# Kernel tuning notes

Hardware: AMD Instinct MI355X
Metric: run time of the kernel (lower is better)

## Reference

```python
import jax, jax.numpy as jnp
import numpy as np

# config (matches init_kwargs)
NA, NEN = 8, 8            # n_agents, n_enemies
NENT = NA + NEN           # n_entities
NFA, NFE = 64, 64         # state_nf_al, state_nf_en
E, A, M, HE = 64, 64, 32, 64  # entity_embed, attn_embed, mixing_embed, hypernet_embed
TD, TE = 64, 64           # task_repre_dim, task_repre_embed_dim
BS, SL = 64, 512


def setup_inputs() -> dict:
    key = jax.random.key(0)
    ks = iter(jax.random.split(key, 32))
    def rn(shape, scale=0.05):
        return jax.random.normal(next(ks), shape, dtype=jnp.float32) * scale
    return {
        "agent_qs": rn((BS, SL, NA), 1.0),
        "states": rn((BS, SL, NA * NFA + NEN * NFE), 1.0),
        "task_repre_mu": rn((BS, SL, NA, TD), 1.0),
        "ally_w": rn((NFA, E)), "ally_b": rn((E,)),
        "enemy_w": rn((NFE, E)), "enemy_b": rn((E,)),
        "q_w": rn((E, A)), "q_b": rn((A,)),
        "k_w": rn((E, A)), "k_b": rn((A,)),
        "hw1_w1": rn((E + NFA + TE, HE)), "hw1_b1": rn((HE,)),
        "hw1_w2": rn((HE, M)), "hw1_b2": rn((M,)),
        "hwf_w1": rn((E + TE, HE)), "hwf_b1": rn((HE,)),
        "hwf_w2": rn((HE, M)), "hwf_b2": rn((M,)),
        "hb1_w": rn((E + TE, M)), "hb1_b": rn((M,)),
        "v_w1": rn((E + TE, M)), "v_b1": rn((M,)),
        "v_w2": rn((M, 1)), "v_b2": rn((1,)),
        "tre_w": rn((TD, TE)), "tre_b": rn((TE,)),
    }


def reference(agent_qs, states, task_repre_mu,
              ally_w, ally_b, enemy_w, enemy_b,
              q_w, q_b, k_w, k_b,
              hw1_w1, hw1_b1, hw1_w2, hw1_b2,
              hwf_w1, hwf_b1, hwf_w2, hwf_b2,
              hb1_w, hb1_b, v_w1, v_b1, v_w2, v_b2,
              tre_w, tre_b):
    bs, sl = agent_qs.shape[:2]
    # decompose_state (state_last_action=False, state_timestep_number=False)
    ally = states[..., : NA * NFA].reshape(bs, sl, NA, NFA)      # [bs,sl,NA,NFA]
    enemy = states[..., NA * NFA:].reshape(bs, sl, NEN, NFE)     # [bs,sl,NEN,NFE]
    ally_e = ally @ ally_w + ally_b                              # [bs,sl,NA,E]
    enemy_e = enemy @ enemy_w + enemy_b                          # [bs,sl,NEN,E]
    ent = jnp.concatenate([ally_e, enemy_e], axis=2)             # [bs,sl,NENT,E]
    q = ent @ q_w + q_b                                          # [bs,sl,NENT,A]
    k = ent @ k_w + k_b
    energy = jnp.einsum('bsqa,bska->bsqk', q, k)                 # [bs,sl,NENT,NENT]
    # torch: F.softmax(energy, dim=1) on [B,n_ent,n_ent] -> softmax over query axis
    attn = jax.nn.softmax(energy, axis=2)
    # attn_out = bmm(value[B,E,n], attn[B,n,n]).mean(-1)
    attn_out = jnp.einsum('bsne,bsnk->bse', ent, attn) / NENT    # [bs,sl,E]

    mean_mu = task_repre_mu.mean(axis=-2)                        # [bs,sl,TD]
    tre = task_repre_mu @ tre_w + tre_b                          # [bs,sl,NA,TE]
    mean_tre = mean_mu @ tre_w + tre_b                           # [bs,sl,TE]

    ent_mix = jnp.concatenate([
        jnp.broadcast_to(attn_out[:, :, None, :], (bs, sl, NA, E)),
        ally, tre], axis=-1)                                     # [bs,sl,NA,E+NFA+TE]
    mix = jnp.concatenate([attn_out, mean_tre], axis=-1)         # [bs,sl,E+TE]

    w1 = jnp.abs(jax.nn.relu(ent_mix @ hw1_w1 + hw1_b1) @ hw1_w2 + hw1_b2)  # [bs,sl,NA,M]
    b1 = mix @ hb1_w + hb1_b                                     # [bs,sl,M]
    hidden = jax.nn.elu(jnp.einsum('bsn,bsnm->bsm', agent_qs, w1) + b1)     # [bs,sl,M]
    wf = jnp.abs(jax.nn.relu(mix @ hwf_w1 + hwf_b1) @ hwf_w2 + hwf_b2)      # [bs,sl,M]
    v = jax.nn.relu(mix @ v_w1 + v_b1) @ v_w2 + v_b2             # [bs,sl,1]
    q_tot = jnp.einsum('bsm,bsm->bs', hidden, wf)[..., None] + v # [bs,sl,1]
    return q_tot
```

## Files before the change

kernel.cpp:

```cpp
#include <hip/hip_runtime.h>
#include <math.h>


#define TOKS 32768

typedef __attribute__((ext_vector_type(8))) short short8;
typedef __attribute__((ext_vector_type(4))) float f32x4;

#define MFMA(a, b, c) __builtin_amdgcn_mfma_f32_16x16x32_bf16((a), (b), (c), 0, 0, 0)

#define E_CAT   0
#define E_WQKT  8192
#define E_ZBRT  13312
#define E_H1T   29696
#define E_W2T   41984
#define E_WFT   44032
#define E_BF16_TOTAL 46080
#define E_AO_US 46464

__device__ __forceinline__ unsigned short bfr(float x) {
    unsigned u = __builtin_bit_cast(unsigned, x);
    u += 0x7fffu + ((u >> 16) & 1u);
    return (unsigned short)(u >> 16);
}
__device__ __forceinline__ float bf2f(unsigned short h) {
    unsigned u = ((unsigned)h) << 16;
    return __builtin_bit_cast(float, u);
}
__device__ __forceinline__ short8 cvt8v(float4 a, float4 b) {
    short8 r;
    r[0] = (short)bfr(a.x); r[1] = (short)bfr(a.y);
    r[2] = (short)bfr(a.z); r[3] = (short)bfr(a.w);
    r[4] = (short)bfr(b.x); r[5] = (short)bfr(b.y);
    r[6] = (short)bfr(b.z); r[7] = (short)bfr(b.w);
    return r;
}
#define SWZ64(r, c)  ((((r) * 64)  + (c)) ^ (((r) & 7) << 3))
#define SWZ128(r, c) ((((r) * 128) + (c)) ^ (((r) & 7) << 3))
#define SWZ192(r, c) ((((r) * 192) + (c)) ^ (((r) & 7) << 3))

__global__ __launch_bounds__(256) void qmix_setup(
    const float* __restrict__ ally_w, const float* __restrict__ enemy_w,
    const float* __restrict__ q_w, const float* __restrict__ k_w,
    const float* __restrict__ k_b,
    const float* __restrict__ hw1_w1, const float* __restrict__ hw1_b1,
    const float* __restrict__ hw1_w2,
    const float* __restrict__ hwf_w1, const float* __restrict__ hwf_b1,
    const float* __restrict__ hwf_w2,
    const float* __restrict__ hb1_w, const float* __restrict__ hb1_b,
    const float* __restrict__ v_w1, const float* __restrict__ v_b1,
    const float* __restrict__ tre_w, const float* __restrict__ tre_b,
    unsigned short* __restrict__ wsb, float* __restrict__ wsf)
{
    int gid = blockIdx.x * 256 + threadIdx.x;
    if (gid < E_BF16_TOTAL) {
        float v = 0.f;
        int base, r, c, K;
        if (gid < E_WQKT) {
            base = E_CAT; K = 128;
            int i = gid - base; r = i >> 7; c = i & 127;
            v = (c < 64) ? ally_w[c * 64 + r] : enemy_w[(c - 64) * 64 + r];
        } else if (gid < E_ZBRT) {
            base = E_WQKT; K = 64;
            int i = gid - base; r = i >> 6; c = i & 63;
            if (r < 64) {
                for (int g = 0; g < 64; ++g) v += q_w[c * 64 + g] * k_w[r * 64 + g];
            } else if (r == 64) {
                for (int g = 0; g < 64; ++g) v += q_w[c * 64 + g] * k_b[g];
            }
        } else if (gid < E_H1T) {
            base = E_ZBRT; K = 128;
            int i = gid - base; r = i >> 7; c = i & 127;
            if (r < 64) {
                if (c < 64) v = hwf_w1[c * 64 + r];
                else for (int g = 0; g < 64; ++g) v += tre_w[(c - 64) * 64 + g] * hwf_w1[(64 + g) * 64 + r];
            } else if (r < 96) {
                int m = r - 64;
                if (c < 64) v = hb1_w[c * 32 + m];
                else for (int g = 0; g < 64; ++g) v += tre_w[(c - 64) * 64 + g] * hb1_w[(64 + g) * 32 + m];
            } else {
                int m = r - 96;
                if (c < 64) v = v_w1[c * 32 + m];
                else for (int g = 0; g < 64; ++g) v += tre_w[(c - 64) * 64 + g] * v_w1[(64 + g) * 32 + m];
            }
        } else if (gid < E_W2T) {
            base = E_H1T; K = 192;
            int i = gid - base; r = i / 192; c = i % 192;
            if (c < 64) v = hw1_w1[(64 + c) * 64 + r];
            else if (c < 128) {
                for (int g = 0; g < 64; ++g) v += tre_w[(c - 64) * 64 + g] * hw1_w1[(128 + g) * 64 + r];
            } else v = hw1_w1[(c - 128) * 64 + r];
        } else if (gid < E_WFT) {
            base = E_W2T; K = 64;
            int i = gid - base; r = i >> 6; c = i & 63;
            v = hw1_w2[c * 32 + r];
        } else {
            base = E_WFT; K = 64;
            int i = gid - base; r = i >> 6; c = i & 63;
            v = hwf_w2[c * 32 + r];
        }
        wsb[base + ((r * K + c) ^ ((r & 7) << 3))] = bfr(v);
    } else if (gid < E_BF16_TOTAL + 192) {
        int j = gid - E_BF16_TOTAL; float v;
        if (j < 64) {
            v = hw1_b1[j];
            for (int g = 0; g < 64; ++g) v += tre_b[g] * hw1_w1[(128 + g) * 64 + j];
        } else if (j < 128) {
            int e = j - 64; v = hwf_b1[e];
            for (int g = 0; g < 64; ++g) v += tre_b[g] * hwf_w1[(64 + g) * 64 + e];
        } else if (j < 160) {
            int m = j - 128; v = hb1_b[m];
            for (int g = 0; g < 64; ++g) v += tre_b[g] * hb1_w[(64 + g) * 32 + m];
        } else {
            int m = j - 160; v = v_b1[m];
            for (int g = 0; g < 64; ++g) v += tre_b[g] * v_w1[(64 + g) * 32 + m];
        }
        wsf[j] = v;
    }
}

__global__ __launch_bounds__(512) void qmix_attn(
    const float* __restrict__ states,
    const float* __restrict__ ally_b, const float* __restrict__ enemy_b,
    const unsigned short* __restrict__ wsb,
    unsigned short* __restrict__ aoG)
{
    __shared__ unsigned short sWa[13312];
    __shared__ unsigned short sE[8][1024];
    __shared__ unsigned short sT[8][1024];

    const int lane = threadIdx.x & 63;
    const int wv   = threadIdx.x >> 6;
    const int l15  = lane & 15;
    const int lg   = lane >> 4;
    const int kb   = lg * 8;
    const size_t t = (size_t)blockIdx.x * 8 + wv;

    const short8 zero8 = {0, 0, 0, 0, 0, 0, 0, 0};
    const f32x4  zero4 = {0.f, 0.f, 0.f, 0.f};

    for (int i = threadIdx.x * 8; i < 13312; i += 512 * 8)
        *(short8*)(sWa + i) = *(const short8*)(wsb + E_CAT + i);

    const int roff = (l15 < 8) ? (l15 * 64 + kb) : (512 + (l15 - 8) * 64 + kb);
    const float* p = states + t * 1024 + roff;
    float4 cur0 = *(const float4*)(p);
    float4 cur1 = *(const float4*)(p + 4);
    float4 cur2 = *(const float4*)(p + 32);
    float4 cur3 = *(const float4*)(p + 36);

    float biasEnt[4];
    #pragma unroll
    for (int nt = 0; nt < 4; ++nt) {
        int col = nt * 16 + l15;
        biasEnt[nt] = (lg < 2) ? ally_b[col] : enemy_b[col];
    }
    __syncthreads();
    const unsigned short* lCAT  = sWa;
    const unsigned short* lWQKT = sWa + 8192;

    unsigned short* E = sE[wv];
    unsigned short* T = sT[wv];

    short8 a01 = cvt8v(cur0, cur1);
    short8 a23 = cvt8v(cur2, cur3);
    const bool isally = (l15 < 8);

    f32x4 accB[4] = {zero4, zero4, zero4, zero4};
    #pragma unroll
    for (int ks = 0; ks < 4; ++ks) {
        short8 af;
        if (ks == 0)      af = isally ? a01 : zero8;
        else if (ks == 1) af = isally ? a23 : zero8;
        else if (ks == 2) af = isally ? zero8 : a01;
        else              af = isally ? zero8 : a23;
        #pragma unroll
        for (int nt = 0; nt < 4; ++nt) {
            short8 w = *(const short8*)&lCAT[SWZ128(nt * 16 + l15, ks * 32 + kb)];
            accB[nt] = MFMA(af, w, accB[nt]);
        }
    }
    float entv[4][4];
    #pragma unroll
    for (int nt = 0; nt < 4; ++nt) {
        #pragma unroll
        for (int reg = 0; reg < 4; ++reg) {
            entv[nt][reg] = accB[nt][reg] + biasEnt[nt];
            E[SWZ64(lg * 4 + reg, nt * 16 + l15)] = bfr(entv[nt][reg]);
        }
    }

    f32x4 accC[5] = {zero4, zero4, zero4, zero4, zero4};
    short8 ef0 = *(const short8*)&E[SWZ64(l15, 0 * 32 + kb)];
    short8 ef1 = *(const short8*)&E[SWZ64(l15, 1 * 32 + kb)];
    #pragma unroll
    for (int nt = 0; nt < 5; ++nt) {
        short8 w0 = *(const short8*)&lWQKT[SWZ64(nt * 16 + l15, 0 * 32 + kb)];
        short8 w1 = *(const short8*)&lWQKT[SWZ64(nt * 16 + l15, 1 * 32 + kb)];
        accC[nt] = MFMA(ef0, w0, accC[nt]);
        accC[nt] = MFMA(ef1, w1, accC[nt]);
    }
    const int src = lane & 48;
    float si[4];
    #pragma unroll
    for (int reg = 0; reg < 4; ++reg) si[reg] = __shfl(accC[4][reg], src);
    #pragma unroll
    for (int nt = 0; nt < 4; ++nt)
        #pragma unroll
        for (int reg = 0; reg < 4; ++reg)
            T[SWZ64(lg * 4 + reg, nt * 16 + l15)] = bfr(accC[nt][reg]);

    f32x4 en = zero4;
    {
        short8 ta0 = *(const short8*)&T[SWZ64(l15, 0 * 32 + kb)];
        short8 ta1 = *(const short8*)&T[SWZ64(l15, 1 * 32 + kb)];
        en = MFMA(ta0, ef0, en);
        en = MFMA(ta1, ef1, en);
    }
    #pragma unroll
    for (int reg = 0; reg < 4; ++reg) en[reg] += si[reg];

    float mx = fmaxf(fmaxf(en[0], en[1]), fmaxf(en[2], en[3]));
    mx = fmaxf(mx, __shfl_xor(mx, 16));
    mx = fmaxf(mx, __shfl_xor(mx, 32));
    float p0 = __expf(en[0] - mx), p1 = __expf(en[1] - mx);
    float p2 = __expf(en[2] - mx), p3 = __expf(en[3] - mx);
    float s = p0 + p1 + p2 + p3;
    s += __shfl_xor(s, 16);
    s += __shfl_xor(s, 32);
    float inv = 1.f / s;
    float r0 = p0 * inv, r1 = p1 * inv, r2 = p2 * inv, r3 = p3 * inv;
    r0 += __shfl_xor(r0, 1); r0 += __shfl_xor(r0, 2); r0 += __shfl_xor(r0, 4); r0 += __shfl_xor(r0, 8);
    r1 += __shfl_xor(r1, 1); r1 += __shfl_xor(r1, 2); r1 += __shfl_xor(r1, 4); r1 += __shfl_xor(r1, 8);
    r2 += __shfl_xor(r2, 1); r2 += __shfl_xor(r2, 2); r2 += __shfl_xor(r2, 4); r2 += __shfl_xor(r2, 8);
    r3 += __shfl_xor(r3, 1); r3 += __shfl_xor(r3, 2); r3 += __shfl_xor(r3, 4); r3 += __shfl_xor(r3, 8);

    float part[4];
    #pragma unroll
    for (int nt = 0; nt < 4; ++nt) {
        float pp = r0 * entv[nt][0] + r1 * entv[nt][1]
                 + r2 * entv[nt][2] + r3 * entv[nt][3];
        pp += __shfl_xor(pp, 16);
        pp += __shfl_xor(pp, 32);
        part[nt] = pp;
    }
    float ao = (lg == 0) ? part[0] : (lg == 1) ? part[1]
             : (lg == 2) ? part[2] : part[3];
    aoG[t * 64 + lane] = bfr(ao * 0.0625f);
}

__device__ __forceinline__ short8 mmfrag(const float* __restrict__ mp) {
    float a0 = 0.f, a1 = 0.f, a2 = 0.f, a3 = 0.f, a4 = 0.f, a5 = 0.f, a6 = 0.f, a7 = 0.f;
    #pragma unroll
    for (int a = 0; a < 8; ++a) {
        float4 u = *(const float4*)(mp + a * 64);
        float4 v = *(const float4*)(mp + a * 64 + 4);
        a0 += u.x; a1 += u.y; a2 += u.z; a3 += u.w;
        a4 += v.x; a5 += v.y; a6 += v.z; a7 += v.w;
    }
    return cvt8v(make_float4(a0 * 0.125f, a1 * 0.125f, a2 * 0.125f, a3 * 0.125f),
                 make_float4(a4 * 0.125f, a5 * 0.125f, a6 * 0.125f, a7 * 0.125f));
}

__global__ __launch_bounds__(256) void qmix_hyper(
    const float* __restrict__ agent_qs, const float* __restrict__ states,
    const float* __restrict__ mu,
    const float* __restrict__ v_w2, const float* __restrict__ v_b2,
    const float* __restrict__ hw1_b2, const float* __restrict__ hwf_b2,
    const unsigned short* __restrict__ wsb, const float* __restrict__ wsf,
    const unsigned short* __restrict__ aoG,
    float* __restrict__ out)
{
    __shared__ unsigned short sWb[16384];
    __shared__ unsigned short sZ[4][1024];
    __shared__ unsigned short sH1[4][2048];
    __shared__ float sB1[4][512];
    __shared__ float sWF[4][512];
    __shared__ float sV[4][16];

    const int lane = threadIdx.x & 63;
    const int wv   = threadIdx.x >> 6;
    const int l15  = lane & 15;
    const int lg   = lane >> 4;
    const int kb   = lg * 8;
    const int T0   = blockIdx.x * 64 + wv * 16;

    const float* BHF = wsf + 64;
    const float* BB1 = wsf + 128;
    const float* BV  = wsf + 160;
    const float* BH1 = wsf + 0;

    const f32x4 zero4 = {0.f, 0.f, 0.f, 0.f};

    for (int i = threadIdx.x * 8; i < 16384; i += 256 * 8)
        *(short8*)(sWb + i) = *(const short8*)(wsb + E_ZBRT + i);
    __syncthreads();

    f32x4 zb[8] = {zero4, zero4, zero4, zero4, zero4, zero4, zero4, zero4};
    #pragma unroll
    for (int ks = 0; ks < 4; ++ks) {
        short8 af;
        if (ks < 2)
            af = *(const short8*)&aoG[(size_t)(T0 + l15) * 64 + ks * 32 + kb];
        else
            af = mmfrag(mu + (size_t)(T0 + l15) * 512 + (ks - 2) * 32 + kb);
        #pragma unroll
        for (int nt = 0; nt < 8; ++nt) {
            short8 w = *(const short8*)&sWb[SWZ128(nt * 16 + l15, ks * 32 + kb)];
            zb[nt] = MFMA(af, w, zb[nt]);
        }
    }
    __syncthreads();

    for (int i = threadIdx.x * 8; i < 16384; i += 256 * 8)
        *(short8*)(sWb + i) = *(const short8*)(wsb + E_H1T + i);

    #pragma unroll
    for (int nt = 0; nt < 4; ++nt) {
        int col = nt * 16 + l15;
        float bz = BHF[col];
        #pragma unroll
        for (int reg = 0; reg < 4; ++reg)
            sZ[wv][SWZ64(lg * 4 + reg, col)] = bfr(fmaxf(zb[nt][reg] + bz, 0.f));
    }
    #pragma unroll
    for (int nt = 4; nt < 6; ++nt) {
        int m = (nt - 4) * 16 + l15;
        float bb = BB1[m];
        #pragma unroll
        for (int reg = 0; reg < 4; ++reg)
            sB1[wv][(lg * 4 + reg) * 32 + m] = zb[nt][reg] + bb;
    }
    {
        float bv0 = BV[l15], bv1 = BV[16 + l15];
        float vw0 = v_w2[l15], vw1 = v_w2[16 + l15];
        #pragma unroll
        for (int reg = 0; reg < 4; ++reg) {
            float vp = fmaxf(zb[6][reg] + bv0, 0.f) * vw0
                     + fmaxf(zb[7][reg] + bv1, 0.f) * vw1;
            vp += __shfl_xor(vp, 1); vp += __shfl_xor(vp, 2);
            vp += __shfl_xor(vp, 4); vp += __shfl_xor(vp, 8);
            if (l15 == 0) sV[wv][lg * 4 + reg] = vp;
        }
    }
    __syncthreads();
    const unsigned short* lH1T = sWb;
    const unsigned short* lW2T = sWb + 12288;
    const unsigned short* lWFT = sWb + 14336;

    {
        f32x4 wfa = zero4, wfb = zero4;
        #pragma unroll
        for (int ks = 0; ks < 2; ++ks) {
            short8 af = *(const short8*)&sZ[wv][SWZ64(l15, ks * 32 + kb)];
            short8 b0 = *(const short8*)&lWFT[SWZ64(l15, ks * 32 + kb)];
            short8 b1 = *(const short8*)&lWFT[SWZ64(16 + l15, ks * 32 + kb)];
            wfa = MFMA(af, b0, wfa);
            wfb = MFMA(af, b1, wfb);
        }
        float hb0 = hwf_b2[l15], hb1 = hwf_b2[16 + l15];
        #pragma unroll
        for (int reg = 0; reg < 4; ++reg) {
            int tok = lg * 4 + reg;
            sWF[wv][tok * 32 + l15]      = fabsf(wfa[reg] + hb0);
            sWF[wv][tok * 32 + 16 + l15] = fabsf(wfb[reg] + hb1);
        }
    }

    const float vb2 = v_b2[0];
    const float b20 = hw1_b2[l15], b21 = hw1_b2[16 + l15];
    const int agent = l15 & 7;

    for (int c = 0; c < 4; ++c) {
        f32x4 h[2][4] = {{zero4, zero4, zero4, zero4}, {zero4, zero4, zero4, zero4}};
        #pragma unroll
        for (int ks = 0; ks < 6; ++ks) {
            #pragma unroll
            for (int ff = 0; ff < 2; ++ff) {
                const size_t tok = (size_t)(T0 + c * 4 + ff * 2 + (l15 >> 3));
                short8 af;
                if (ks < 2)
                    af = cvt8v(*(const float4*)(states + tok * 1024 + agent * 64 + ks * 32 + kb),
                               *(const float4*)(states + tok * 1024 + agent * 64 + ks * 32 + kb + 4));
                else if (ks < 4)
                    af = cvt8v(*(const float4*)(mu + tok * 512 + agent * 64 + (ks - 2) * 32 + kb),
                               *(const float4*)(mu + tok * 512 + agent * 64 + (ks - 2) * 32 + kb + 4));
                else
                    af = *(const short8*)&aoG[tok * 64 + (ks - 4) * 32 + kb];
                #pragma unroll
                for (int nt = 0; nt < 4; ++nt) {
                    short8 w = *(const short8*)&lH1T[SWZ192(nt * 16 + l15, ks * 32 + kb)];
                    h[ff][nt] = MFMA(af, w, h[ff][nt]);
                }
            }
        }
        #pragma unroll
        for (int ff = 0; ff < 2; ++ff)
            #pragma unroll
            for (int nt = 0; nt < 4; ++nt) {
                int col = nt * 16 + l15;
                float bh = BH1[col];
                #pragma unroll
                for (int reg = 0; reg < 4; ++reg)
                    sH1[wv][SWZ64(ff * 16 + lg * 4 + reg, col)] =
                        bfr(fmaxf(h[ff][nt][reg] + bh, 0.f));
            }

        f32x4 wa[2] = {zero4, zero4}, wb[2] = {zero4, zero4};
        #pragma unroll
        for (int ks = 0; ks < 2; ++ks) {
            short8 b0 = *(const short8*)&lW2T[SWZ64(l15, ks * 32 + kb)];
            short8 b1 = *(const short8*)&lW2T[SWZ64(16 + l15, ks * 32 + kb)];
            #pragma unroll
            for (int ff = 0; ff < 2; ++ff) {
                short8 af = *(const short8*)&sH1[wv][SWZ64(ff * 16 + l15, ks * 32 + kb)];
                wa[ff] = MFMA(af, b0, wa[ff]);
                wb[ff] = MFMA(af, b1, wb[ff]);
            }
        }

        #pragma unroll
        for (int ff = 0; ff < 2; ++ff) {
            const int tokL = c * 4 + ff * 2 + (lg >> 1);
            float hp0 = 0.f, hp1 = 0.f;
            #pragma unroll
            for (int reg = 0; reg < 4; ++reg) {
                float qsv = agent_qs[(size_t)(T0 + tokL) * 8 + (lg & 1) * 4 + reg];
                hp0 += qsv * fabsf(wa[ff][reg] + b20);
                hp1 += qsv * fabsf(wb[ff][reg] + b21);
            }
            hp0 += __shfl_xor(hp0, 16);
            hp1 += __shfl_xor(hp1, 16);
            float e0 = hp0 + sB1[wv][tokL * 32 + l15];
            float e1 = hp1 + sB1[wv][tokL * 32 + 16 + l15];
            float hid0 = e0 > 0.f ? e0 : (__expf(e0) - 1.f);
            float hid1 = e1 > 0.f ? e1 : (__expf(e1) - 1.f);
            float q = hid0 * sWF[wv][tokL * 32 + l15]
                    + hid1 * sWF[wv][tokL * 32 + 16 + l15];
            q += __shfl_xor(q, 1); q += __shfl_xor(q, 2);
            q += __shfl_xor(q, 4); q += __shfl_xor(q, 8);
            if (l15 == 0 && (lg & 1) == 0)
                out[T0 + tokL] = q + sV[wv][tokL] + vb2;
        }
    }
}

extern "C" void kernel_launch(void* const* d_in, const int* in_sizes, int n_in,
                              void* d_out, int out_size, void* d_ws, size_t ws_size,
                              hipStream_t stream)
{
    const float* agent_qs = (const float*)d_in[0];
    const float* states   = (const float*)d_in[1];
    const float* mu       = (const float*)d_in[2];
    const float* ally_w   = (const float*)d_in[3];
    const float* ally_b   = (const float*)d_in[4];
    const float* enemy_w  = (const float*)d_in[5];
    const float* enemy_b  = (const float*)d_in[6];
    const float* q_w      = (const float*)d_in[7];
    const float* k_w      = (const float*)d_in[9];
    const float* k_b      = (const float*)d_in[10];
    const float* hw1_w1   = (const float*)d_in[11];
    const float* hw1_b1   = (const float*)d_in[12];
    const float* hw1_w2   = (const float*)d_in[13];
    const float* hw1_b2   = (const float*)d_in[14];
    const float* hwf_w1   = (const float*)d_in[15];
    const float* hwf_b1   = (const float*)d_in[16];
    const float* hwf_w2   = (const float*)d_in[17];
    const float* hwf_b2   = (const float*)d_in[18];
    const float* hb1_w    = (const float*)d_in[19];
    const float* hb1_b    = (const float*)d_in[20];
    const float* v_w1     = (const float*)d_in[21];
    const float* v_b1     = (const float*)d_in[22];
    const float* v_w2     = (const float*)d_in[23];
    const float* v_b2     = (const float*)d_in[24];
    const float* tre_w    = (const float*)d_in[25];
    const float* tre_b    = (const float*)d_in[26];

    unsigned short* wsb = (unsigned short*)d_ws;
    float* wsf = (float*)((char*)d_ws + (size_t)E_BF16_TOTAL * 2);
    unsigned short* aoG = wsb + E_AO_US;
    float* out = (float*)d_out;

    hipLaunchKernelGGL(qmix_setup, dim3(181), dim3(256), 0, stream,
                       ally_w, enemy_w, q_w, k_w, k_b,
                       hw1_w1, hw1_b1, hw1_w2,
                       hwf_w1, hwf_b1, hwf_w2,
                       hb1_w, hb1_b, v_w1, v_b1, tre_w, tre_b,
                       wsb, wsf);

    hipLaunchKernelGGL(qmix_attn, dim3(TOKS / 8), dim3(512), 0, stream,
                       states, ally_b, enemy_b, wsb, aoG);

    hipLaunchKernelGGL(qmix_hyper, dim3(TOKS / 64), dim3(256), 0, stream,
                       agent_qs, states, mu, v_w2, v_b2, hw1_b2, hwf_b2,
                       wsb, wsf, aoG, out);
}
```

Baseline: 91.36 us.

## Halve tokens per wave in hyper kernel to double grid parallelism

Each wave in the hypernet kernel now handles 8 tokens instead of 16, and the grid doubles from TOKS/64 to TOKS/32 blocks. The mix-stage MFMA uses half-empty 16-row tiles (rows 8-15 zero-padded). The per-chunk loop processes one 16-row agent fragment instead of two, and the Z and H1 shared buffers are merged into one. The aim is more blocks and waves in flight to hide memory latency and less LDS use per block. The cost is wasted MFMA work on the padded rows and the 32 KB weight staging into LDS being repeated twice as often across the grid.

```diff
diff --git a/kernel.cpp b/kernel.cpp
--- a/kernel.cpp
+++ b/kernel.cpp
@@ -272,38 +272,41 @@
     float* __restrict__ out)
 {
     __shared__ unsigned short sWb[16384];
-    __shared__ unsigned short sZ[4][1024];
-    __shared__ unsigned short sH1[4][2048];
-    __shared__ float sB1[4][512];
-    __shared__ float sWF[4][512];
-    __shared__ float sV[4][16];
+    __shared__ unsigned short sZH[4][1024];
+    __shared__ float sB1[4][256];
+    __shared__ float sWF[4][256];
+    __shared__ float sV[4][8];
 
     const int lane = threadIdx.x & 63;
     const int wv   = threadIdx.x >> 6;
     const int l15  = lane & 15;
     const int lg   = lane >> 4;
     const int kb   = lg * 8;
-    const int T0   = blockIdx.x * 64 + wv * 16;
-
+    const int T0   = blockIdx.x * 32 + wv * 8;
+
+    const float* BH1 = wsf + 0;
     const float* BHF = wsf + 64;
     const float* BB1 = wsf + 128;
     const float* BV  = wsf + 160;
-    const float* BH1 = wsf + 0;
-
-    const f32x4 zero4 = {0.f, 0.f, 0.f, 0.f};
+
+    const short8 zero8 = {0, 0, 0, 0, 0, 0, 0, 0};
+    const f32x4  zero4 = {0.f, 0.f, 0.f, 0.f};
+
+    for (int i = lane; i < 512; i += 64) sZH[wv][512 + i] = 0;
 
     for (int i = threadIdx.x * 8; i < 16384; i += 256 * 8)
         *(short8*)(sWb + i) = *(const short8*)(wsb + E_ZBRT + i);
     __syncthreads();
 
     f32x4 zb[8] = {zero4, zero4, zero4, zero4, zero4, zero4, zero4, zero4};
+    const bool arow = (l15 < 8);
     #pragma unroll
     for (int ks = 0; ks < 4; ++ks) {
         short8 af;
         if (ks < 2)
-            af = *(const short8*)&aoG[(size_t)(T0 + l15) * 64 + ks * 32 + kb];
+            af = arow ? *(const short8*)&aoG[(size_t)(T0 + l15) * 64 + ks * 32 + kb] : zero8;
         else
-            af = mmfrag(mu + (size_t)(T0 + l15) * 512 + (ks - 2) * 32 + kb);
+            af = arow ? mmfrag(mu + (size_t)(T0 + l15) * 512 + (ks - 2) * 32 + kb) : zero8;
         #pragma unroll
         for (int nt = 0; nt < 8; ++nt) {
             short8 w = *(const short8*)&sWb[SWZ128(nt * 16 + l15, ks * 32 + kb)];
@@ -315,21 +318,23 @@
     for (int i = threadIdx.x * 8; i < 16384; i += 256 * 8)
         *(short8*)(sWb + i) = *(const short8*)(wsb + E_H1T + i);
 
-    #pragma unroll
-    for (int nt = 0; nt < 4; ++nt) {
-        int col = nt * 16 + l15;
-        float bz = BHF[col];
-        #pragma unroll
-        for (int reg = 0; reg < 4; ++reg)
-            sZ[wv][SWZ64(lg * 4 + reg, col)] = bfr(fmaxf(zb[nt][reg] + bz, 0.f));
-    }
-    #pragma unroll
-    for (int nt = 4; nt < 6; ++nt) {
-        int m = (nt - 4) * 16 + l15;
-        float bb = BB1[m];
-        #pragma unroll
-        for (int reg = 0; reg < 4; ++reg)
-            sB1[wv][(lg * 4 + reg) * 32 + m] = zb[nt][reg] + bb;
+    if (lg < 2) {
+        #pragma unroll
+        for (int nt = 0; nt < 4; ++nt) {
+            int col = nt * 16 + l15;
+            float bz = BHF[col];
+            #pragma unroll
+            for (int reg = 0; reg < 4; ++reg)
+                sZH[wv][SWZ64(lg * 4 + reg, col)] = bfr(fmaxf(zb[nt][reg] + bz, 0.f));
+        }
+        #pragma unroll
+        for (int nt = 4; nt < 6; ++nt) {
+            int m = (nt - 4) * 16 + l15;
+            float bb = BB1[m];
+            #pragma unroll
+            for (int reg = 0; reg < 4; ++reg)
+                sB1[wv][(lg * 4 + reg) * 32 + m] = zb[nt][reg] + bb;
+        }
     }
     {
         float bv0 = BV[l15], bv1 = BV[16 + l15];
@@ -340,7 +345,7 @@
                      + fmaxf(zb[7][reg] + bv1, 0.f) * vw1;
             vp += __shfl_xor(vp, 1); vp += __shfl_xor(vp, 2);
             vp += __shfl_xor(vp, 4); vp += __shfl_xor(vp, 8);
-            if (l15 == 0) sV[wv][lg * 4 + reg] = vp;
+            if (l15 == 0 && lg < 2) sV[wv][lg * 4 + reg] = vp;
         }
     }
     __syncthreads();
@@ -352,18 +357,20 @@
         f32x4 wfa = zero4, wfb = zero4;
         #pragma unroll
         for (int ks = 0; ks < 2; ++ks) {
-            short8 af = *(const short8*)&sZ[wv][SWZ64(l15, ks * 32 + kb)];
+            short8 af = *(const short8*)&sZH[wv][SWZ64(l15, ks * 32 + kb)];
             short8 b0 = *(const short8*)&lWFT[SWZ64(l15, ks * 32 + kb)];
             short8 b1 = *(const short8*)&lWFT[SWZ64(16 + l15, ks * 32 + kb)];
             wfa = MFMA(af, b0, wfa);
             wfb = MFMA(af, b1, wfb);
         }
-        float hb0 = hwf_b2[l15], hb1 = hwf_b2[16 + l15];
-        #pragma unroll
-        for (int reg = 0; reg < 4; ++reg) {
-            int tok = lg * 4 + reg;
-            sWF[wv][tok * 32 + l15]      = fabsf(wfa[reg] + hb0);
-            sWF[wv][tok * 32 + 16 + l15] = fabsf(wfb[reg] + hb1);
+        if (lg < 2) {
+            float hb0 = hwf_b2[l15], hb1 = hwf_b2[16 + l15];
+            #pragma unroll
+            for (int reg = 0; reg < 4; ++reg) {
+                int tok = lg * 4 + reg;
+                sWF[wv][tok * 32 + l15]      = fabsf(wfa[reg] + hb0);
+                sWF[wv][tok * 32 + 16 + l15] = fabsf(wfb[reg] + hb1);
+            }
         }
     }
 
@@ -372,76 +379,65 @@
     const int agent = l15 & 7;
 
     for (int c = 0; c < 4; ++c) {
-        f32x4 h[2][4] = {{zero4, zero4, zero4, zero4}, {zero4, zero4, zero4, zero4}};
+        const size_t tokA = (size_t)(T0 + c * 2 + (l15 >> 3));
+        f32x4 h[4] = {zero4, zero4, zero4, zero4};
         #pragma unroll
         for (int ks = 0; ks < 6; ++ks) {
-            #pragma unroll
-            for (int ff = 0; ff < 2; ++ff) {
-                const size_t tok = (size_t)(T0 + c * 4 + ff * 2 + (l15 >> 3));
-                short8 af;
-                if (ks < 2)
-                    af = cvt8v(*(const float4*)(states + tok * 1024 + agent * 64 + ks * 32 + kb),
-                               *(const float4*)(states + tok * 1024 + agent * 64 + ks * 32 + kb + 4));
-                else if (ks < 4)
-                    af = cvt8v(*(const float4*)(mu + tok * 512 + agent * 64 + (ks - 2) * 32 + kb),
-                               *(const float4*)(mu + tok * 512 + agent * 64 + (ks - 2) * 32 + kb + 4));
-                else
-                    af = *(const short8*)&aoG[tok * 64 + (ks - 4) * 32 + kb];
-                #pragma unroll
-                for (int nt = 0; nt < 4; ++nt) {
-                    short8 w = *(const short8*)&lH1T[SWZ192(nt * 16 + l15, ks * 32 + kb)];
-                    h[ff][nt] = MFMA(af, w, h[ff][nt]);
-                }
-            }
-        }
-        #pragma unroll
-        for (int ff = 0; ff < 2; ++ff)
+            short8 af;
+            if (ks < 2)
+                af = cvt8v(*(const float4*)(states + tokA * 1024 + agent * 64 + ks * 32 + kb),
+                           *(const float4*)(states + tokA * 1024 + agent * 64 + ks * 32 + kb + 4));
+            else if (ks < 4)
+                af = cvt8v(*(const float4*)(mu + tokA * 512 + agent * 64 + (ks - 2) * 32 + kb),
+                           *(const float4*)(mu + tokA * 512 + agent * 64 + (ks - 2) * 32 + kb + 4));
+            else
+                af = *(const short8*)&aoG[tokA * 64 + (ks - 4) * 32 + kb];
             #pragma unroll
             for (int nt = 0; nt < 4; ++nt) {
-                int col = nt * 16 + l15;
-                float bh = BH1[col];
-                #pragma unroll
-                for (int reg = 0; reg < 4; ++reg)
-                    sH1[wv][SWZ64(ff * 16 + lg * 4 + reg, col)] =
-                        bfr(fmaxf(h[ff][nt][reg] + bh, 0.f));
+                short8 w = *(const short8*)&lH1T[SWZ192(nt * 16 + l15, ks * 32 + kb)];
+                h[nt] = MFMA(af, w, h[nt]);
             }
-
-        f32x4 wa[2] = {zero4, zero4}, wb[2] = {zero4, zero4};
+        }
+        #pragma unroll
+        for (int nt = 0; nt < 4; ++nt) {
+            int col = nt * 16 + l15;
+            float bh = BH1[col];
+            #pragma unroll
+            for (int reg = 0; reg < 4; ++reg)
+                sZH[wv][SWZ64(lg * 4 + reg, col)] = bfr(fmaxf(h[nt][reg] + bh, 0.f));
+        }
+
+        f32x4 wa = zero4, wb = zero4;
         #pragma unroll
         for (int ks = 0; ks < 2; ++ks) {
+            short8 af = *(const short8*)&sZH[wv][SWZ64(l15, ks * 32 + kb)];
             short8 b0 = *(const short8*)&lW2T[SWZ64(l15, ks * 32 + kb)];
             short8 b1 = *(const short8*)&lW2T[SWZ64(16 + l15, ks * 32 + kb)];
-            #pragma unroll
-            for (int ff = 0; ff < 2; ++ff) {
-                short8 af = *(const short8*)&sH1[wv][SWZ64(ff * 16 + l15, ks * 32 + kb)];
-                wa[ff] = MFMA(af, b0, wa[ff]);
-                wb[ff] = MFMA(af, b1, wb[ff]);
-            }
-        }
-
-        #pragma unroll
-        for (int ff = 0; ff < 2; ++ff) {
-            const int tokL = c * 4 + ff * 2 + (lg >> 1);
-            float hp0 = 0.f, hp1 = 0.f;
-            #pragma unroll
-            for (int reg = 0; reg < 4; ++reg) {
-                float qsv = agent_qs[(size_t)(T0 + tokL) * 8 + (lg & 1) * 4 + reg];
-                hp0 += qsv * fabsf(wa[ff][reg] + b20);
-                hp1 += qsv * fabsf(wb[ff][reg] + b21);
-            }
-            hp0 += __shfl_xor(hp0, 16);
-            hp1 += __shfl_xor(hp1, 16);
-            float e0 = hp0 + sB1[wv][tokL * 32 + l15];
-            float e1 = hp1 + sB1[wv][tokL * 32 + 16 + l15];
-            float hid0 = e0 > 0.f ? e0 : (__expf(e0) - 1.f);
-            float hid1 = e1 > 0.f ? e1 : (__expf(e1) - 1.f);
-            float q = hid0 * sWF[wv][tokL * 32 + l15]
-                    + hid1 * sWF[wv][tokL * 32 + 16 + l15];
-            q += __shfl_xor(q, 1); q += __shfl_xor(q, 2);
-            q += __shfl_xor(q, 4); q += __shfl_xor(q, 8);
-            if (l15 == 0 && (lg & 1) == 0)
-                out[T0 + tokL] = q + sV[wv][tokL] + vb2;
-        }
+            wa = MFMA(af, b0, wa);
+            wb = MFMA(af, b1, wb);
+        }
+
+        float hp0 = 0.f, hp1 = 0.f;
+        #pragma unroll
+        for (int reg = 0; reg < 4; ++reg) {
+            int row = lg * 4 + reg;
+            float qsv = agent_qs[(size_t)(T0 + c * 2 + (row >> 3)) * 8 + (row & 7)];
+            hp0 += qsv * fabsf(wa[reg] + b20);
+            hp1 += qsv * fabsf(wb[reg] + b21);
+        }
+        hp0 += __shfl_xor(hp0, 16);
+        hp1 += __shfl_xor(hp1, 16);
+        int tokL = c * 2 + (lg >> 1);
+        float e0 = hp0 + sB1[wv][tokL * 32 + l15];
+        float e1 = hp1 + sB1[wv][tokL * 32 + 16 + l15];
+        float hid0 = e0 > 0.f ? e0 : (__expf(e0) - 1.f);
+        float hid1 = e1 > 0.f ? e1 : (__expf(e1) - 1.f);
+        float q = hid0 * sWF[wv][tokL * 32 + l15]
+                + hid1 * sWF[wv][tokL * 32 + 16 + l15];
+        q += __shfl_xor(q, 1); q += __shfl_xor(q, 2);
+        q += __shfl_xor(q, 4); q += __shfl_xor(q, 8);
+        if (l15 == 0 && (lg & 1) == 0)
+            out[T0 + tokL] = q + sV[wv][tokL] + vb2;
     }
 }
 
@@ -491,7 +487,7 @@
     hipLaunchKernelGGL(qmix_attn, dim3(TOKS / 8), dim3(512), 0, stream,
                        states, ally_b, enemy_b, wsb, aoG);
 
-    hipLaunchKernelGGL(qmix_hyper, dim3(TOKS / 64), dim3(256), 0, stream,
+    hipLaunchKernelGGL(qmix_hyper, dim3(TOKS / 32), dim3(256), 0, stream,
                        agent_qs, states, mu, v_w2, v_b2, hw1_b2, hwf_b2,
                        wsb, wsf, aoG, out);
 }
```

After: 116.0 us. 27.0% more time.

## Prefetch next token pair's inputs in hyper loop and stage mean-mu via LDS

Applied to the files above, without the earlier changes.

The main hyper-network loop now processes two tokens per iteration and software-prefetches the states, mu and attention-output fragments for the next iteration into registers, so global loads overlap with MFMA work. The mean over agents of task_repre_mu is now computed cooperatively by the whole block with coalesced loads and staged in shared memory, replacing the per-lane strided mmfrag gather. The first attention-output fragments are also loaded before the weight-staging barrier. This costs more registers, which may reduce occupancy.

```diff
diff --git a/kernel.cpp b/kernel.cpp
--- a/kernel.cpp
+++ b/kernel.cpp
@@ -249,19 +249,6 @@
     aoG[t * 64 + lane] = bfr(ao * 0.0625f);
 }
 
-__device__ __forceinline__ short8 mmfrag(const float* __restrict__ mp) {
-    float a0 = 0.f, a1 = 0.f, a2 = 0.f, a3 = 0.f, a4 = 0.f, a5 = 0.f, a6 = 0.f, a7 = 0.f;
-    #pragma unroll
-    for (int a = 0; a < 8; ++a) {
-        float4 u = *(const float4*)(mp + a * 64);
-        float4 v = *(const float4*)(mp + a * 64 + 4);
-        a0 += u.x; a1 += u.y; a2 += u.z; a3 += u.w;
-        a4 += v.x; a5 += v.y; a6 += v.z; a7 += v.w;
-    }
-    return cvt8v(make_float4(a0 * 0.125f, a1 * 0.125f, a2 * 0.125f, a3 * 0.125f),
-                 make_float4(a4 * 0.125f, a5 * 0.125f, a6 * 0.125f, a7 * 0.125f));
-}
-
 __global__ __launch_bounds__(256) void qmix_hyper(
     const float* __restrict__ agent_qs, const float* __restrict__ states,
     const float* __restrict__ mu,
@@ -273,37 +260,63 @@
 {
     __shared__ unsigned short sWb[16384];
     __shared__ unsigned short sZ[4][1024];
-    __shared__ unsigned short sH1[4][2048];
+    __shared__ unsigned short sH1all[8192];
     __shared__ float sB1[4][512];
     __shared__ float sWF[4][512];
     __shared__ float sV[4][16];
 
-    const int lane = threadIdx.x & 63;
-    const int wv   = threadIdx.x >> 6;
+    const int tid  = threadIdx.x;
+    const int lane = tid & 63;
+    const int wv   = tid >> 6;
     const int l15  = lane & 15;
     const int lg   = lane >> 4;
     const int kb   = lg * 8;
     const int T0   = blockIdx.x * 64 + wv * 16;
-
+    const int tokB = blockIdx.x * 64;
+
+    const float* BH1 = wsf + 0;
     const float* BHF = wsf + 64;
     const float* BB1 = wsf + 128;
     const float* BV  = wsf + 160;
-    const float* BH1 = wsf + 0;
 
     const f32x4 zero4 = {0.f, 0.f, 0.f, 0.f};
 
-    for (int i = threadIdx.x * 8; i < 16384; i += 256 * 8)
+    for (int i = tid * 8; i < 16384; i += 256 * 8)
         *(short8*)(sWb + i) = *(const short8*)(wsb + E_ZBRT + i);
+
+    short8 zA0 = *(const short8*)&aoG[(size_t)(T0 + l15) * 64 + kb];
+    short8 zA1 = *(const short8*)&aoG[(size_t)(T0 + l15) * 64 + 32 + kb];
+
+    #pragma unroll
+    for (int tg = 0; tg < 64; tg += 32) {
+        int tok = tg + (tid >> 3);
+        int e8  = (tid & 7) * 8;
+        const float* mp = mu + (size_t)(tokB + tok) * 512 + e8;
+        float s0 = 0.f, s1 = 0.f, s2 = 0.f, s3 = 0.f,
+              s4 = 0.f, s5 = 0.f, s6 = 0.f, s7 = 0.f;
+        #pragma unroll
+        for (int a = 0; a < 8; ++a) {
+            float4 u = *(const float4*)(mp + a * 64);
+            float4 v = *(const float4*)(mp + a * 64 + 4);
+            s0 += u.x; s1 += u.y; s2 += u.z; s3 += u.w;
+            s4 += v.x; s5 += v.y; s6 += v.z; s7 += v.w;
+        }
+        short8 r;
+        r[0] = (short)bfr(s0 * 0.125f); r[1] = (short)bfr(s1 * 0.125f);
+        r[2] = (short)bfr(s2 * 0.125f); r[3] = (short)bfr(s3 * 0.125f);
+        r[4] = (short)bfr(s4 * 0.125f); r[5] = (short)bfr(s5 * 0.125f);
+        r[6] = (short)bfr(s6 * 0.125f); r[7] = (short)bfr(s7 * 0.125f);
+        *(short8*)&sH1all[SWZ64(tok, e8)] = r;
+    }
     __syncthreads();
 
     f32x4 zb[8] = {zero4, zero4, zero4, zero4, zero4, zero4, zero4, zero4};
     #pragma unroll
     for (int ks = 0; ks < 4; ++ks) {
         short8 af;
-        if (ks < 2)
-            af = *(const short8*)&aoG[(size_t)(T0 + l15) * 64 + ks * 32 + kb];
-        else
-            af = mmfrag(mu + (size_t)(T0 + l15) * 512 + (ks - 2) * 32 + kb);
+        if (ks == 0)      af = zA0;
+        else if (ks == 1) af = zA1;
+        else af = *(const short8*)&sH1all[SWZ64(wv * 16 + l15, (ks - 2) * 32 + kb)];
         #pragma unroll
         for (int nt = 0; nt < 8; ++nt) {
             short8 w = *(const short8*)&sWb[SWZ128(nt * 16 + l15, ks * 32 + kb)];
@@ -312,7 +325,7 @@
     }
     __syncthreads();
 
-    for (int i = threadIdx.x * 8; i < 16384; i += 256 * 8)
+    for (int i = tid * 8; i < 16384; i += 256 * 8)
         *(short8*)(sWb + i) = *(const short8*)(wsb + E_H1T + i);
 
     #pragma unroll
@@ -347,6 +360,7 @@
     const unsigned short* lH1T = sWb;
     const unsigned short* lW2T = sWb + 12288;
     const unsigned short* lWFT = sWb + 14336;
+    unsigned short* tile = sH1all + wv * 2048;
 
     {
         f32x4 wfa = zero4, wfb = zero4;
@@ -370,78 +384,91 @@
     const float vb2 = v_b2[0];
     const float b20 = hw1_b2[l15], b21 = hw1_b2[16 + l15];
     const int agent = l15 & 7;
-
-    for (int c = 0; c < 4; ++c) {
-        f32x4 h[2][4] = {{zero4, zero4, zero4, zero4}, {zero4, zero4, zero4, zero4}};
+    const int toff  = l15 >> 3;
+
+    float4 cs0, cs1, cs2, cs3, cm0, cm1, cm2, cm3;
+    short8 ca0, ca1;
+    {
+        const size_t tokA = (size_t)(T0 + toff);
+        const float* sp = states + tokA * 1024 + agent * 64 + kb;
+        const float* mp = mu + tokA * 512 + agent * 64 + kb;
+        cs0 = *(const float4*)sp;        cs1 = *(const float4*)(sp + 4);
+        cs2 = *(const float4*)(sp + 32); cs3 = *(const float4*)(sp + 36);
+        cm0 = *(const float4*)mp;        cm1 = *(const float4*)(mp + 4);
+        cm2 = *(const float4*)(mp + 32); cm3 = *(const float4*)(mp + 36);
+        ca0 = *(const short8*)&aoG[tokA * 64 + kb];
+        ca1 = *(const short8*)&aoG[tokA * 64 + 32 + kb];
+    }
+
+    for (int mc = 0; mc < 8; ++mc) {
+        float4 us0 = cs0, us1 = cs1, us2 = cs2, us3 = cs3;
+        float4 um0 = cm0, um1 = cm1, um2 = cm2, um3 = cm3;
+        short8 ua0 = ca0, ua1 = ca1;
+        if (mc < 7) {
+            const size_t tokA = (size_t)(T0 + (mc + 1) * 2 + toff);
+            const float* sp = states + tokA * 1024 + agent * 64 + kb;
+            const float* mp = mu + tokA * 512 + agent * 64 + kb;
+            cs0 = *(const float4*)sp;        cs1 = *(const float4*)(sp + 4);
+            cs2 = *(const float4*)(sp + 32); cs3 = *(const float4*)(sp + 36);
+            cm0 = *(const float4*)mp;        cm1 = *(const float4*)(mp + 4);
+            cm2 = *(const float4*)(mp + 32); cm3 = *(const float4*)(mp + 36);
+            ca0 = *(const short8*)&aoG[tokA * 64 + kb];
+            ca1 = *(const short8*)&aoG[tokA * 64 + 32 + kb];
+        }
+        short8 f0 = cvt8v(us0, us1), f1 = cvt8v(us2, us3);
+        short8 f2 = cvt8v(um0, um1), f3 = cvt8v(um2, um3);
+
+        f32x4 h[4] = {zero4, zero4, zero4, zero4};
         #pragma unroll
         for (int ks = 0; ks < 6; ++ks) {
-            #pragma unroll
-            for (int ff = 0; ff < 2; ++ff) {
-                const size_t tok = (size_t)(T0 + c * 4 + ff * 2 + (l15 >> 3));
-                short8 af;
-                if (ks < 2)
-                    af = cvt8v(*(const float4*)(states + tok * 1024 + agent * 64 + ks * 32 + kb),
-                               *(const float4*)(states + tok * 1024 + agent * 64 + ks * 32 + kb + 4));
-                else if (ks < 4)
-                    af = cvt8v(*(const float4*)(mu + tok * 512 + agent * 64 + (ks - 2) * 32 + kb),
-                               *(const float4*)(mu + tok * 512 + agent * 64 + (ks - 2) * 32 + kb + 4));
-                else
-                    af = *(const short8*)&aoG[tok * 64 + (ks - 4) * 32 + kb];
-                #pragma unroll
-                for (int nt = 0; nt < 4; ++nt) {
-                    short8 w = *(const short8*)&lH1T[SWZ192(nt * 16 + l15, ks * 32 + kb)];
-                    h[ff][nt] = MFMA(af, w, h[ff][nt]);
-                }
-            }
-        }
-        #pragma unroll
-        for (int ff = 0; ff < 2; ++ff)
+            short8 af = (ks == 0) ? f0 : (ks == 1) ? f1 : (ks == 2) ? f2
+                      : (ks == 3) ? f3 : (ks == 4) ? ua0 : ua1;
             #pragma unroll
             for (int nt = 0; nt < 4; ++nt) {
-                int col = nt * 16 + l15;
-                float bh = BH1[col];
-                #pragma unroll
-                for (int reg = 0; reg < 4; ++reg)
-                    sH1[wv][SWZ64(ff * 16 + lg * 4 + reg, col)] =
-                        bfr(fmaxf(h[ff][nt][reg] + bh, 0.f));
+                short8 w = *(const short8*)&lH1T[SWZ192(nt * 16 + l15, ks * 32 + kb)];
+                h[nt] = MFMA(af, w, h[nt]);
             }
-
-        f32x4 wa[2] = {zero4, zero4}, wb[2] = {zero4, zero4};
+        }
+        #pragma unroll
+        for (int nt = 0; nt < 4; ++nt) {
+            int col = nt * 16 + l15;
+            float bh = BH1[col];
+            #pragma unroll
+            for (int reg = 0; reg < 4; ++reg)
+                tile[SWZ64(lg * 4 + reg, col)] = bfr(fmaxf(h[nt][reg] + bh, 0.f));
+        }
+
+        f32x4 wa = zero4, wb = zero4;
         #pragma unroll
         for (int ks = 0; ks < 2; ++ks) {
+            short8 af = *(const short8*)&tile[SWZ64(l15, ks * 32 + kb)];
             short8 b0 = *(const short8*)&lW2T[SWZ64(l15, ks * 32 + kb)];
             short8 b1 = *(const short8*)&lW2T[SWZ64(16 + l15, ks * 32 + kb)];
-            #pragma unroll
-            for (int ff = 0; ff < 2; ++ff) {
-                short8 af = *(const short8*)&sH1[wv][SWZ64(ff * 16 + l15, ks * 32 + kb)];
-                wa[ff] = MFMA(af, b0, wa[ff]);
-                wb[ff] = MFMA(af, b1, wb[ff]);
-            }
-        }
-
-        #pragma unroll
-        for (int ff = 0; ff < 2; ++ff) {
-            const int tokL = c * 4 + ff * 2 + (lg >> 1);
-            float hp0 = 0.f, hp1 = 0.f;
-            #pragma unroll
-            for (int reg = 0; reg < 4; ++reg) {
-                float qsv = agent_qs[(size_t)(T0 + tokL) * 8 + (lg & 1) * 4 + reg];
-                hp0 += qsv * fabsf(wa[ff][reg] + b20);
-                hp1 += qsv * fabsf(wb[ff][reg] + b21);
-            }
-            hp0 += __shfl_xor(hp0, 16);
-            hp1 += __shfl_xor(hp1, 16);
-            float e0 = hp0 + sB1[wv][tokL * 32 + l15];
-            float e1 = hp1 + sB1[wv][tokL * 32 + 16 + l15];
-            float hid0 = e0 > 0.f ? e0 : (__expf(e0) - 1.f);
-            float hid1 = e1 > 0.f ? e1 : (__expf(e1) - 1.f);
-            float q = hid0 * sWF[wv][tokL * 32 + l15]
-                    + hid1 * sWF[wv][tokL * 32 + 16 + l15];
-            q += __shfl_xor(q, 1); q += __shfl_xor(q, 2);
-            q += __shfl_xor(q, 4); q += __shfl_xor(q, 8);
-            if (l15 == 0 && (lg & 1) == 0)
-                out[T0 + tokL] = q + sV[wv][tokL] + vb2;
-        }
+            wa = MFMA(af, b0, wa);
+            wb = MFMA(af, b1, wb);
+        }
+
+        float hp0 = 0.f, hp1 = 0.f;
+        #pragma unroll
+        for (int reg = 0; reg < 4; ++reg) {
+            int row = lg * 4 + reg;
+            float qsv = agent_qs[(size_t)(T0 + mc * 2 + (row >> 3)) * 8 + (row & 7)];
+            hp0 += qsv * fabsf(wa[reg] + b20);
+            hp1 += qsv * fabsf(wb[reg] + b21);
+        }
+        hp0 += __shfl_xor(hp0, 16);
+        hp1 += __shfl_xor(hp1, 16);
+        int tokL = mc * 2 + (lg >> 1);
+        float e0 = hp0 + sB1[wv][tokL * 32 + l15];
+        float e1 = hp1 + sB1[wv][tokL * 32 + 16 + l15];
+        float hid0 = e0 > 0.f ? e0 : (__expf(e0) - 1.f);
+        float hid1 = e1 > 0.f ? e1 : (__expf(e1) - 1.f);
+        float q = hid0 * sWF[wv][tokL * 32 + l15]
+                + hid1 * sWF[wv][tokL * 32 + 16 + l15];
+        q += __shfl_xor(q, 1); q += __shfl_xor(q, 2);
+        q += __shfl_xor(q, 4); q += __shfl_xor(q, 8);
+        if (l15 == 0 && (lg & 1) == 0)
+            out[T0 + tokL] = q + sV[wv][tokL] + vb2;
     }
 }
 
```

After: 94.23 us. +3.1%, slower.
